# Kernel tuning notes

Hardware: AMD Instinct MI355X
Metric: run time of the kernel (lower is better)

The kernel has to match this reference:

```python
import jax, jax.numpy as jnp
import numpy as np

B, N, D, E, H = 4, 1024, 1024, 8, 4096


def setup_inputs() -> dict:
    key = jax.random.key(0)
    ks = jax.random.split(key, 8)
    x = jax.random.normal(ks[0], (B, N, D), dtype=jnp.float32)
    # gumbel noise, matching F.gumbel_softmax's -log(-log(U))
    u = jax.random.uniform(ks[1], (B * N, E), dtype=jnp.float32, minval=1e-9, maxval=1.0)
    gumbel = -jnp.log(-jnp.log(u))
    router_w = jax.random.normal(ks[2], (D, E), dtype=jnp.float32) * 0.02
    router_b = jnp.zeros((E,), dtype=jnp.float32)
    w1 = jax.random.normal(ks[3], (E, D, H), dtype=jnp.float32) * 0.02
    b1 = jnp.zeros((E, H), dtype=jnp.float32)
    w2 = jax.random.normal(ks[4], (E, H, D), dtype=jnp.float32) * 0.02
    b2 = jnp.zeros((E, D), dtype=jnp.float32)
    return {"x": x, "gumbel": gumbel, "router_w": router_w, "router_b": router_b,
            "w1": w1, "b1": b1, "w2": w2, "b2": b2}


def reference(x, gumbel, router_w, router_b, w1, b1, w2, b2):
    b, n, d = x.shape
    e = router_w.shape[1]
    xf = x.reshape(-1, d)                      # (T, D), T = B*N tokens
    logits = xf @ router_w + router_b          # (T, E)

    # hard gumbel-softmax with straight-through estimator (tau = 1.0)
    y_soft = jax.nn.softmax(logits + gumbel, axis=-1)
    hard = jax.nn.one_hot(jnp.argmax(y_soft, axis=-1), e, dtype=y_soft.dtype)
    weights = hard - jax.lax.stop_gradient(y_soft) + y_soft   # (T, E)

    # load-balancing aux loss
    probs = jax.nn.softmax(logits, axis=-1)
    count = jnp.maximum(jnp.float32(xf.shape[0]), 1.0)
    importance = probs.sum(axis=0) / count
    aux_loss = jnp.mean((importance - 1.0 / e) ** 2)

    # dense all-expert FFN: every expert processes every token
    hidden = jax.nn.gelu(jnp.einsum('td,edh->eth', xf, w1) + b1[:, None, :],
                         approximate=False)                    # (E, T, H)
    expert_out = jnp.einsum('eth,ehd->etd', hidden, w2) + b2[:, None, :]  # (E, T, D)

    # weighted combine (einsum 'ej,ejd->jd' in the original)
    out = jnp.einsum('te,etd->td', weights, expert_out)        # (T, D)
    return out.reshape(b, n, d), aux_loss
```

## Files before the change

### kernel.cpp

```cpp
#include <hip/hip_runtime.h>
#include <math.h>

#define T_TOK 4096
#define D_DIM 1024

typedef __attribute__((ext_vector_type(4))) float f32x4;
typedef __attribute__((ext_vector_type(8))) short s16x8;

__device__ __forceinline__ unsigned short f2bf(float f){
  union { float f; unsigned u; } v; v.f = f;
  unsigned r = v.u + 0x7FFFu + ((v.u >> 16) & 1u);
  return (unsigned short)(r >> 16);
}

__device__ __forceinline__ void gld_lds16(const unsigned short* g, unsigned short* l){
  __builtin_amdgcn_global_load_lds(
      (const __attribute__((address_space(1))) unsigned int*)g,
      (__attribute__((address_space(3))) unsigned int*)l, 16, 0, 0);
}

__global__ __launch_bounds__(256) void router_kernel(
    const float* __restrict__ x, const float* __restrict__ gumbel,
    const float* __restrict__ rw, const float* __restrict__ rb,
    int* __restrict__ expert_id, float* __restrict__ wtok,
    double* __restrict__ prob_sums, int* __restrict__ counts)
{
  int wave = threadIdx.x >> 6, lane = threadIdx.x & 63;
  int t = blockIdx.x * 4 + wave;
  const float* xr = x + (size_t)t * D_DIM;
  double acc[8];
  #pragma unroll
  for (int e = 0; e < 8; e++) acc[e] = 0.0;
  #pragma unroll
  for (int i = 0; i < 16; i++){
    int d = i * 64 + lane;
    double xv = (double)xr[d];
    const float4* rwp = (const float4*)(rw + (size_t)d * 8);
    float4 r0 = rwp[0], r1 = rwp[1];
    acc[0] += xv * (double)r0.x; acc[1] += xv * (double)r0.y;
    acc[2] += xv * (double)r0.z; acc[3] += xv * (double)r0.w;
    acc[4] += xv * (double)r1.x; acc[5] += xv * (double)r1.y;
    acc[6] += xv * (double)r1.z; acc[7] += xv * (double)r1.w;
  }
  #pragma unroll
  for (int e = 0; e < 8; e++){
    #pragma unroll
    for (int off = 32; off; off >>= 1) acc[e] += __shfl_xor(acc[e], off);
  }
  double logit[8], z[8];
  #pragma unroll
  for (int e = 0; e < 8; e++){
    logit[e] = acc[e] + (double)rb[e];
    z[e] = logit[e] + (double)gumbel[(size_t)t * 8 + e];
  }
  int amax = 0;
  #pragma unroll
  for (int e = 1; e < 8; e++) if (z[e] > z[amax]) amax = e;
  float zm = (float)z[amax];
  float se = 0.f;
  #pragma unroll
  for (int e = 0; e < 8; e++) se += expf((float)z[e] - zm);
  float y = 1.f / se;
  float w = (1.0f - y) + y;
  double lm = logit[0];
  #pragma unroll
  for (int e = 1; e < 8; e++) lm = fmax(lm, logit[e]);
  float p[8]; float ps = 0.f;
  #pragma unroll
  for (int e = 0; e < 8; e++){ p[e] = expf((float)(logit[e] - lm)); ps += p[e]; }
  float inv = 1.f / ps;

  __shared__ float sprob[4][8];
  if (lane == 0){
    expert_id[t] = amax; wtok[t] = w;
    atomicAdd(&counts[amax], 1);
    #pragma unroll
    for (int e = 0; e < 8; e++) sprob[wave][e] = p[e] * inv;
  }
  __syncthreads();
  if (threadIdx.x < 8){
    double s = (double)sprob[0][threadIdx.x] + (double)sprob[1][threadIdx.x]
             + (double)sprob[2][threadIdx.x] + (double)sprob[3][threadIdx.x];
    atomicAdd(&prob_sums[threadIdx.x], s);
  }
}

__global__ void finalize_kernel(const double* __restrict__ prob_sums, const int* __restrict__ counts,
                                int* __restrict__ offsets, int* __restrict__ cursor,
                                float* __restrict__ aux_out)
{
  if (threadIdx.x == 0){
    int off = 0; double aux = 0.0;
    for (int e = 0; e < 8; e++){ offsets[e] = off; cursor[e] = off; off += counts[e]; }
    for (int e = 0; e < 8; e++){
      double imp = prob_sums[e] / 4096.0;
      double d = imp - 0.125;
      aux += d * d;
    }
    aux_out[0] = (float)(aux / 8.0);
  }
}

__global__ __launch_bounds__(256) void scatter_kernel(
    const float* __restrict__ x, const int* __restrict__ expert_id, const float* __restrict__ wtok,
    int* __restrict__ cursor, int* __restrict__ token_of, float* __restrict__ gw,
    unsigned short* __restrict__ Xg)
{
  int t = blockIdx.x;
  __shared__ int spos;
  if (threadIdx.x == 0){
    int e = expert_id[t];
    int p = atomicAdd(&cursor[e], 1);
    spos = p;
    token_of[p] = t; gw[p] = wtok[t];
  }
  __syncthreads();
  int pos = spos;
  float4 v = ((const float4*)(x + (size_t)t * D_DIM))[threadIdx.x];
  ushort4 o; o.x = f2bf(v.x); o.y = f2bf(v.y); o.z = f2bf(v.z); o.w = f2bf(v.w);
  ((ushort4*)(Xg + (size_t)pos * D_DIM))[threadIdx.x] = o;
}

__global__ __launch_bounds__(256) void transpose_w(
    const float* __restrict__ W, unsigned short* __restrict__ WT, int K, int N)
{
  int e = blockIdx.z;
  int k0 = blockIdx.x * 64;
  int n0 = blockIdx.y * 64;
  __shared__ float tile[64][65];
  const float* src = W + (size_t)e * K * N;
  int tid = threadIdx.x;
  int r = tid >> 4;
  int c4 = (tid & 15) * 4;
  #pragma unroll
  for (int j = 0; j < 4; j++){
    int k = r + j * 16;
    float4 v = *(const float4*)(src + (size_t)(k0 + k) * N + n0 + c4);
    tile[k][c4] = v.x; tile[k][c4 + 1] = v.y; tile[k][c4 + 2] = v.z; tile[k][c4 + 3] = v.w;
  }
  __syncthreads();
  unsigned short* dst = WT + (size_t)e * N * K;
  int n = tid >> 2;
  #pragma unroll
  for (int h = 0; h < 2; h++){
    int s = (tid & 3) + h * 4;
    unsigned short buf[8];
    #pragma unroll
    for (int j = 0; j < 8; j++) buf[j] = f2bf(tile[s * 8 + j][n]);
    *(s16x8*)(dst + (size_t)(n0 + n) * K + k0 + s * 8) = *(s16x8*)buf;
  }
}

template<int K, int N, int PASS2>
__global__ __launch_bounds__(256) void ffn_gemm(
    const unsigned short* __restrict__ A,
    const unsigned short* __restrict__ BT,
    const float* __restrict__ bias,
    const int* __restrict__ counts, const int* __restrict__ offsets,
    const int* __restrict__ token_of, const float* __restrict__ gw,
    unsigned short* __restrict__ Hout,
    float* __restrict__ Fout)
{
  int e = blockIdx.z;
  int cnt = counts[e];
  int by = blockIdx.y;
  if (by * 128 >= cnt) return;
  int offs = offsets[e];
  int bx = blockIdx.x;
  int tid = threadIdx.x;
  int lane = tid & 63;
  int wv = __builtin_amdgcn_readfirstlane(tid >> 6);
  int wm = wv & 1, wn = wv >> 1;

  __shared__ unsigned short sA[128 * 32];
  __shared__ unsigned short sB[128 * 32];

  size_t aoff[2], boff[2];
  unsigned short *aldst[2], *bldst[2];
  #pragma unroll
  for (int j = 0; j < 2; j++){
    int c = 2 * wv + j;
    int row = c * 16 + (lane >> 2);
    int pos = offs + by * 128 + row;
    if (pos > T_TOK - 1) pos = T_TOK - 1;
    aoff[j] = (size_t)pos * K + (lane & 3) * 8;
    aldst[j] = &sA[c * 512];
    int n = bx * 128 + c * 16 + (lane >> 2);
    boff[j] = ((size_t)e * N + n) * K + (lane & 3) * 8;
    bldst[j] = &sB[c * 512];
  }

  f32x4 accv[4][4];
  #pragma unroll
  for (int mi = 0; mi < 4; mi++)
    #pragma unroll
    for (int ni = 0; ni < 4; ni++) accv[mi][ni] = (f32x4){0.f, 0.f, 0.f, 0.f};

  int col = lane & 15, quad = lane >> 4;
  const int NK = K / 32;
  for (int kt = 0; kt < NK; ++kt){
    __syncthreads();
    #pragma unroll
    for (int j = 0; j < 2; j++) gld_lds16(A + aoff[j] + kt * 32, aldst[j]);
    #pragma unroll
    for (int j = 0; j < 2; j++) gld_lds16(BT + boff[j] + kt * 32, bldst[j]);
    __syncthreads();
    s16x8 af[4], bf[4];
    #pragma unroll
    for (int mi = 0; mi < 4; mi++)
      af[mi] = *(const s16x8*)&sA[(wm * 64 + mi * 16 + col) * 32 + quad * 8];
    #pragma unroll
    for (int ni = 0; ni < 4; ni++)
      bf[ni] = *(const s16x8*)&sB[(wn * 64 + ni * 16 + col) * 32 + quad * 8];
    #pragma unroll
    for (int mi = 0; mi < 4; mi++)
      #pragma unroll
      for (int ni = 0; ni < 4; ni++)
        accv[mi][ni] = __builtin_amdgcn_mfma_f32_16x16x32_bf16(af[mi], bf[ni], accv[mi][ni], 0, 0, 0);
  }

  float bv[4];
  #pragma unroll
  for (int ni = 0; ni < 4; ni++)
    bv[ni] = bias[(size_t)e * N + bx * 128 + wn * 64 + ni * 16 + col];

  if (PASS2 == 0){
    #pragma unroll
    for (int mi = 0; mi < 4; mi++){
      int rbase = by * 128 + wm * 64 + mi * 16 + quad * 4;
      #pragma unroll
      for (int r = 0; r < 4; r++){
        int row = rbase + r;
        if (row < cnt){
          size_t orow = (size_t)(offs + row) * N + bx * 128 + wn * 64 + col;
          #pragma unroll
          for (int ni = 0; ni < 4; ni++){
            float v = accv[mi][ni][r] + bv[ni];
            float g = 0.5f * v * (1.0f + erff(v * 0.70710678118654752f));
            Hout[orow + ni * 16] = f2bf(g);
          }
        }
      }
    }
  } else {
    #pragma unroll
    for (int mi = 0; mi < 4; mi++){
      int rbase = by * 128 + wm * 64 + mi * 16 + quad * 4;
      #pragma unroll
      for (int r = 0; r < 4; r++){
        int row = rbase + r;
        if (row < cnt){
          int pos = offs + row;
          int tok = token_of[pos];
          float wgt = gw[pos];
          size_t orow = (size_t)tok * N + bx * 128 + wn * 64 + col;
          #pragma unroll
          for (int ni = 0; ni < 4; ni++)
            Fout[orow + ni * 16] = (accv[mi][ni][r] + bv[ni]) * wgt;
        }
      }
    }
  }
}

extern "C" void kernel_launch(void* const* d_in, const int* in_sizes, int n_in,
                              void* d_out, int out_size, void* d_ws, size_t ws_size,
                              hipStream_t stream)
{
  const float* x      = (const float*)d_in[0];
  const float* gumbel = (const float*)d_in[1];
  const float* rw     = (const float*)d_in[2];
  const float* rb     = (const float*)d_in[3];
  const float* w1     = (const float*)d_in[4];
  const float* b1     = (const float*)d_in[5];
  const float* w2     = (const float*)d_in[6];
  const float* b2     = (const float*)d_in[7];
  float* out = (float*)d_out;

  char* ws = (char*)d_ws;
  double* prob_sums = (double*)(ws + 0);
  int* counts    = (int*)(ws + 64);
  int* offsets   = (int*)(ws + 96);
  int* cursor    = (int*)(ws + 128);
  int* expert_id = (int*)(ws + 256);
  float* wtok    = (float*)(ws + 256 + 16384);
  int* token_of  = (int*)(ws + 256 + 2 * 16384);
  float* gw      = (float*)(ws + 256 + 3 * 16384);
  unsigned short* Xg     = (unsigned short*)(ws + 65792);
  unsigned short* hidden = (unsigned short*)(ws + 65792 + 8388608);
  unsigned short* wT     = (unsigned short*)(ws + 65792 + 8388608 + 33554432);

  hipMemsetAsync(ws, 0, 256, stream);

  router_kernel<<<1024, 256, 0, stream>>>(x, gumbel, rw, rb, expert_id, wtok, prob_sums, counts);
  finalize_kernel<<<1, 64, 0, stream>>>(prob_sums, counts, offsets, cursor, out + 4194304);
  scatter_kernel<<<4096, 256, 0, stream>>>(x, expert_id, wtok, cursor, token_of, gw, Xg);

  transpose_w<<<dim3(16, 64, 8), 256, 0, stream>>>(w1, wT, 1024, 4096);
  ffn_gemm<1024, 4096, 0><<<dim3(32, 32, 8), 256, 0, stream>>>(
      Xg, wT, b1, counts, offsets, nullptr, nullptr, hidden, nullptr);

  transpose_w<<<dim3(64, 16, 8), 256, 0, stream>>>(w2, wT, 4096, 1024);
  ffn_gemm<4096, 1024, 1><<<dim3(8, 32, 8), 256, 0, stream>>>(
      hidden, wT, b2, counts, offsets, token_of, gw, nullptr, out);
}
```

Baseline: 591.4 us.

## Split-K second FFN GEMM with atomics, double-buffer it, fuse router with w1 transpose

The second expert GEMM is split into two K halves, and each half atomically accumulates into a pre-zeroed output, so more blocks can fill the GPU. That kernel also double-buffers its LDS tiles so the next global-to-LDS load overlaps the current MFMA work. The router and the w1 transpose are merged into one launch so the two independent jobs run concurrently. In exchange it adds an output memset and atomic traffic, and float summation order becomes nondeterministic.

```diff
diff --git a/kernel.cpp b/kernel.cpp
--- a/kernel.cpp
+++ b/kernel.cpp
@@ -19,14 +19,16 @@
       (__attribute__((address_space(3))) unsigned int*)l, 16, 0, 0);
 }
 
-__global__ __launch_bounds__(256) void router_kernel(
+__device__ __forceinline__ void router_body(
+    int bid, char* smraw,
     const float* __restrict__ x, const float* __restrict__ gumbel,
     const float* __restrict__ rw, const float* __restrict__ rb,
     int* __restrict__ expert_id, float* __restrict__ wtok,
     double* __restrict__ prob_sums, int* __restrict__ counts)
 {
+  float (*sprob)[8] = (float(*)[8])smraw;
   int wave = threadIdx.x >> 6, lane = threadIdx.x & 63;
-  int t = blockIdx.x * 4 + wave;
+  int t = bid * 4 + wave;
   const float* xr = x + (size_t)t * D_DIM;
   double acc[8];
   #pragma unroll
@@ -70,7 +72,6 @@
   for (int e = 0; e < 8; e++){ p[e] = expf((float)(logit[e] - lm)); ps += p[e]; }
   float inv = 1.f / ps;
 
-  __shared__ float sprob[4][8];
   if (lane == 0){
     expert_id[t] = amax; wtok[t] = w;
     atomicAdd(&counts[amax], 1);
@@ -83,6 +84,61 @@
              + (double)sprob[2][threadIdx.x] + (double)sprob[3][threadIdx.x];
     atomicAdd(&prob_sums[threadIdx.x], s);
   }
+}
+
+__device__ __forceinline__ void transpose_body(
+    const float* __restrict__ W, unsigned short* __restrict__ WT,
+    int K, int N, int e, int kb, int nb, char* smraw)
+{
+  float (*tile)[65] = (float(*)[65])smraw;
+  int k0 = kb * 64, n0 = nb * 64;
+  const float* src = W + (size_t)e * K * N;
+  int tid = threadIdx.x;
+  int r = tid >> 4;
+  int c4 = (tid & 15) * 4;
+  #pragma unroll
+  for (int j = 0; j < 4; j++){
+    int k = r + j * 16;
+    float4 v = *(const float4*)(src + (size_t)(k0 + k) * N + n0 + c4);
+    tile[k][c4] = v.x; tile[k][c4 + 1] = v.y; tile[k][c4 + 2] = v.z; tile[k][c4 + 3] = v.w;
+  }
+  __syncthreads();
+  unsigned short* dst = WT + (size_t)e * N * K;
+  int n = tid >> 2;
+  #pragma unroll
+  for (int h = 0; h < 2; h++){
+    int s = (tid & 3) + h * 4;
+    unsigned short buf[8];
+    #pragma unroll
+    for (int j = 0; j < 8; j++) buf[j] = f2bf(tile[s * 8 + j][n]);
+    *(s16x8*)(dst + (size_t)(n0 + n) * K + k0 + s * 8) = *(s16x8*)buf;
+  }
+}
+
+__global__ __launch_bounds__(256) void prep1_kernel(
+    const float* __restrict__ x, const float* __restrict__ gumbel,
+    const float* __restrict__ rw, const float* __restrict__ rb,
+    int* __restrict__ expert_id, float* __restrict__ wtok,
+    double* __restrict__ prob_sums, int* __restrict__ counts,
+    const float* __restrict__ w1, unsigned short* __restrict__ w1T)
+{
+  __shared__ __align__(16) char smraw[64 * 65 * 4];
+  if (blockIdx.x < 1024){
+    router_body(blockIdx.x, smraw, x, gumbel, rw, rb, expert_id, wtok, prob_sums, counts);
+  } else {
+    int b = blockIdx.x - 1024;
+    int e = b >> 10;
+    int rem = b & 1023;
+    int kb = rem & 15, nb = rem >> 4;
+    transpose_body(w1, w1T, 1024, 4096, e, kb, nb, smraw);
+  }
+}
+
+__global__ __launch_bounds__(256) void transpose_w(
+    const float* __restrict__ W, unsigned short* __restrict__ WT, int K, int N)
+{
+  __shared__ __align__(16) char smraw[64 * 65 * 4];
+  transpose_body(W, WT, K, N, blockIdx.z, blockIdx.x, blockIdx.y, smraw);
 }
 
 __global__ void finalize_kernel(const double* __restrict__ prob_sums, const int* __restrict__ counts,
@@ -121,46 +177,14 @@
   ((ushort4*)(Xg + (size_t)pos * D_DIM))[threadIdx.x] = o;
 }
 
-__global__ __launch_bounds__(256) void transpose_w(
-    const float* __restrict__ W, unsigned short* __restrict__ WT, int K, int N)
-{
-  int e = blockIdx.z;
-  int k0 = blockIdx.x * 64;
-  int n0 = blockIdx.y * 64;
-  __shared__ float tile[64][65];
-  const float* src = W + (size_t)e * K * N;
-  int tid = threadIdx.x;
-  int r = tid >> 4;
-  int c4 = (tid & 15) * 4;
-  #pragma unroll
-  for (int j = 0; j < 4; j++){
-    int k = r + j * 16;
-    float4 v = *(const float4*)(src + (size_t)(k0 + k) * N + n0 + c4);
-    tile[k][c4] = v.x; tile[k][c4 + 1] = v.y; tile[k][c4 + 2] = v.z; tile[k][c4 + 3] = v.w;
-  }
-  __syncthreads();
-  unsigned short* dst = WT + (size_t)e * N * K;
-  int n = tid >> 2;
-  #pragma unroll
-  for (int h = 0; h < 2; h++){
-    int s = (tid & 3) + h * 4;
-    unsigned short buf[8];
-    #pragma unroll
-    for (int j = 0; j < 8; j++) buf[j] = f2bf(tile[s * 8 + j][n]);
-    *(s16x8*)(dst + (size_t)(n0 + n) * K + k0 + s * 8) = *(s16x8*)buf;
-  }
-}
-
-template<int K, int N, int PASS2>
-__global__ __launch_bounds__(256) void ffn_gemm(
+__global__ __launch_bounds__(256) void ffn1_kernel(
     const unsigned short* __restrict__ A,
     const unsigned short* __restrict__ BT,
     const float* __restrict__ bias,
     const int* __restrict__ counts, const int* __restrict__ offsets,
-    const int* __restrict__ token_of, const float* __restrict__ gw,
-    unsigned short* __restrict__ Hout,
-    float* __restrict__ Fout)
-{
+    unsigned short* __restrict__ Hout)
+{
+  const int K = 1024, N = 4096;
   int e = blockIdx.z;
   int cnt = counts[e];
   int by = blockIdx.y;
@@ -185,7 +209,7 @@
     if (pos > T_TOK - 1) pos = T_TOK - 1;
     aoff[j] = (size_t)pos * K + (lane & 3) * 8;
     aldst[j] = &sA[c * 512];
-    int n = bx * 128 + c * 16 + (lane >> 2);
+    int n = bx * 128 + row;
     boff[j] = ((size_t)e * N + n) * K + (lane & 3) * 8;
     bldst[j] = &sB[c * 512];
   }
@@ -224,39 +248,117 @@
   for (int ni = 0; ni < 4; ni++)
     bv[ni] = bias[(size_t)e * N + bx * 128 + wn * 64 + ni * 16 + col];
 
-  if (PASS2 == 0){
-    #pragma unroll
-    for (int mi = 0; mi < 4; mi++){
-      int rbase = by * 128 + wm * 64 + mi * 16 + quad * 4;
-      #pragma unroll
-      for (int r = 0; r < 4; r++){
-        int row = rbase + r;
-        if (row < cnt){
-          size_t orow = (size_t)(offs + row) * N + bx * 128 + wn * 64 + col;
-          #pragma unroll
-          for (int ni = 0; ni < 4; ni++){
-            float v = accv[mi][ni][r] + bv[ni];
-            float g = 0.5f * v * (1.0f + erff(v * 0.70710678118654752f));
-            Hout[orow + ni * 16] = f2bf(g);
-          }
+  #pragma unroll
+  for (int mi = 0; mi < 4; mi++){
+    int rbase = by * 128 + wm * 64 + mi * 16 + quad * 4;
+    #pragma unroll
+    for (int r = 0; r < 4; r++){
+      int row = rbase + r;
+      if (row < cnt){
+        size_t orow = (size_t)(offs + row) * N + bx * 128 + wn * 64 + col;
+        #pragma unroll
+        for (int ni = 0; ni < 4; ni++){
+          float v = accv[mi][ni][r] + bv[ni];
+          float g = 0.5f * v * (1.0f + erff(v * 0.70710678118654752f));
+          Hout[orow + ni * 16] = f2bf(g);
         }
       }
     }
-  } else {
-    #pragma unroll
-    for (int mi = 0; mi < 4; mi++){
-      int rbase = by * 128 + wm * 64 + mi * 16 + quad * 4;
+  }
+}
+
+__global__ __launch_bounds__(256) void ffn2_kernel(
+    const unsigned short* __restrict__ A,
+    const unsigned short* __restrict__ BT,
+    const float* __restrict__ bias,
+    const int* __restrict__ counts, const int* __restrict__ offsets,
+    const int* __restrict__ token_of, const float* __restrict__ gw,
+    float* __restrict__ Fout)
+{
+  const int K = 4096, N = 1024, KL = 2048;
+  int e = blockIdx.z;
+  int cnt = counts[e];
+  int by = blockIdx.y;
+  if (by * 128 >= cnt) return;
+  int offs = offsets[e];
+  int bx = blockIdx.x & 7, ks = blockIdx.x >> 3;
+  int tid = threadIdx.x;
+  int lane = tid & 63;
+  int wv = __builtin_amdgcn_readfirstlane(tid >> 6);
+  int wm = wv & 1, wn = wv >> 1;
+
+  __shared__ unsigned short sA[2][128 * 32];
+  __shared__ unsigned short sB[2][128 * 32];
+
+  size_t aoff[2], boff[2];
+  int ach[2];
+  #pragma unroll
+  for (int j = 0; j < 2; j++){
+    int c = 2 * wv + j;
+    int row = c * 16 + (lane >> 2);
+    int pos = offs + by * 128 + row;
+    if (pos > T_TOK - 1) pos = T_TOK - 1;
+    aoff[j] = (size_t)pos * K + (size_t)ks * KL + (lane & 3) * 8;
+    int n = bx * 128 + row;
+    boff[j] = ((size_t)e * N + n) * K + (size_t)ks * KL + (lane & 3) * 8;
+    ach[j] = c * 512;
+  }
+
+  auto stage = [&](int kt, int b){
+    #pragma unroll
+    for (int j = 0; j < 2; j++) gld_lds16(A + aoff[j] + kt * 32, &sA[b][ach[j]]);
+    #pragma unroll
+    for (int j = 0; j < 2; j++) gld_lds16(BT + boff[j] + kt * 32, &sB[b][ach[j]]);
+  };
+
+  f32x4 accv[4][4];
+  #pragma unroll
+  for (int mi = 0; mi < 4; mi++)
+    #pragma unroll
+    for (int ni = 0; ni < 4; ni++) accv[mi][ni] = (f32x4){0.f, 0.f, 0.f, 0.f};
+
+  stage(0, 0);
+  int col = lane & 15, quad = lane >> 4;
+  const int NK = KL / 32;
+  for (int kt = 0; kt < NK; ++kt){
+    __syncthreads();
+    if (kt + 1 < NK) stage(kt + 1, (kt + 1) & 1);
+    int b = kt & 1;
+    s16x8 af[4], bf[4];
+    #pragma unroll
+    for (int mi = 0; mi < 4; mi++)
+      af[mi] = *(const s16x8*)&sA[b][(wm * 64 + mi * 16 + col) * 32 + quad * 8];
+    #pragma unroll
+    for (int ni = 0; ni < 4; ni++)
+      bf[ni] = *(const s16x8*)&sB[b][(wn * 64 + ni * 16 + col) * 32 + quad * 8];
+    #pragma unroll
+    for (int mi = 0; mi < 4; mi++)
       #pragma unroll
-      for (int r = 0; r < 4; r++){
-        int row = rbase + r;
-        if (row < cnt){
-          int pos = offs + row;
-          int tok = token_of[pos];
-          float wgt = gw[pos];
-          size_t orow = (size_t)tok * N + bx * 128 + wn * 64 + col;
-          #pragma unroll
-          for (int ni = 0; ni < 4; ni++)
-            Fout[orow + ni * 16] = (accv[mi][ni][r] + bv[ni]) * wgt;
+      for (int ni = 0; ni < 4; ni++)
+        accv[mi][ni] = __builtin_amdgcn_mfma_f32_16x16x32_bf16(af[mi], bf[ni], accv[mi][ni], 0, 0, 0);
+  }
+
+  float bv[4];
+  #pragma unroll
+  for (int ni = 0; ni < 4; ni++)
+    bv[ni] = bias[(size_t)e * N + bx * 128 + wn * 64 + ni * 16 + col];
+
+  #pragma unroll
+  for (int mi = 0; mi < 4; mi++){
+    int rbase = by * 128 + wm * 64 + mi * 16 + quad * 4;
+    #pragma unroll
+    for (int r = 0; r < 4; r++){
+      int row = rbase + r;
+      if (row < cnt){
+        int pos = offs + row;
+        int tok = token_of[pos];
+        float wgt = gw[pos];
+        size_t orow = (size_t)tok * N + bx * 128 + wn * 64 + col;
+        #pragma unroll
+        for (int ni = 0; ni < 4; ni++){
+          float v = accv[mi][ni][r];
+          if (ks == 0) v += bv[ni];
+          atomicAdd(&Fout[orow + ni * 16], v * wgt);
         }
       }
     }
@@ -291,16 +393,17 @@
   unsigned short* wT     = (unsigned short*)(ws + 65792 + 8388608 + 33554432);
 
   hipMemsetAsync(ws, 0, 256, stream);
-
-  router_kernel<<<1024, 256, 0, stream>>>(x, gumbel, rw, rb, expert_id, wtok, prob_sums, counts);
+  hipMemsetAsync(out, 0, (size_t)out_size * sizeof(float), stream);
+
+  prep1_kernel<<<9216, 256, 0, stream>>>(x, gumbel, rw, rb, expert_id, wtok,
+                                         prob_sums, counts, w1, wT);
   finalize_kernel<<<1, 64, 0, stream>>>(prob_sums, counts, offsets, cursor, out + 4194304);
   scatter_kernel<<<4096, 256, 0, stream>>>(x, expert_id, wtok, cursor, token_of, gw, Xg);
 
-  transpose_w<<<dim3(16, 64, 8), 256, 0, stream>>>(w1, wT, 1024, 4096);
-  ffn_gemm<1024, 4096, 0><<<dim3(32, 32, 8), 256, 0, stream>>>(
-      Xg, wT, b1, counts, offsets, nullptr, nullptr, hidden, nullptr);
+  ffn1_kernel<<<dim3(32, 32, 8), 256, 0, stream>>>(Xg, wT, b1, counts, offsets, hidden);
 
   transpose_w<<<dim3(64, 16, 8), 256, 0, stream>>>(w2, wT, 4096, 1024);
-  ffn_gemm<4096, 1024, 1><<<dim3(8, 32, 8), 256, 0, stream>>>(
-      hidden, wT, b2, counts, offsets, token_of, gw, nullptr, out);
-}
+
+  ffn2_kernel<<<dim3(16, 32, 8), 256, 0, stream>>>(hidden, wT, b2, counts, offsets,
+                                                   token_of, gw, out);
+}
```

Measured after the change: 595.1 us. Within noise of the previous version (+0.6%).
